# Optimization experiments

Hardware: AMD Instinct MI355X
Metric: run time of the kernel (lower is better)

Reference implementation:

```python
import jax, jax.numpy as jnp
import numpy as np

B, C_IN, H, W = 4, 128, 32, 32
C_SKIP, C_OUT = 64, 64
D_MODEL = 2 * C_SKIP            # 128 (channels after concat)
D_STATE, D_CONV, EXPAND = 16, 4, 2
D_INNER = EXPAND * D_MODEL      # 256
DT_RANK = int(np.ceil(D_MODEL / 16))  # 8
LN_EPS = 1e-5


def setup_inputs() -> dict:
    key = jax.random.key(0)
    ks = jax.random.split(key, 12)
    s = 0.02
    return {
        "x": jax.random.normal(ks[0], (B, C_IN, H, W), jnp.float32),
        "skip_x": jax.random.normal(ks[1], (B, C_SKIP, 2 * H, 2 * W), jnp.float32),
        # ConvTranspose2d(in, skip, k=2, s=2): torch weight layout (in, out, kh, kw)
        "up_w": jax.random.normal(ks[2], (C_IN, C_SKIP, 2, 2), jnp.float32) * s,
        "up_b": jnp.zeros((C_SKIP,), jnp.float32),
        # Mamba params (torch Linear layout: (out_features, in_features))
        "in_proj_w": jax.random.normal(ks[3], (2 * D_INNER, D_MODEL), jnp.float32) * s,
        "conv1d_w": jax.random.normal(ks[4], (D_INNER, 1, D_CONV), jnp.float32) * s,
        "conv1d_b": jnp.zeros((D_INNER,), jnp.float32),
        "x_proj_w": jax.random.normal(ks[5], (DT_RANK + 2 * D_STATE, D_INNER), jnp.float32) * s,
        "dt_proj_w": jax.random.normal(ks[6], (D_INNER, DT_RANK), jnp.float32) * s,
        "dt_proj_b": jnp.zeros((D_INNER,), jnp.float32),
        "A_log": jnp.log(jnp.broadcast_to(jnp.arange(1, D_STATE + 1, dtype=jnp.float32), (D_INNER, D_STATE))),
        "Dp": jnp.ones((D_INNER,), jnp.float32),
        "out_proj_w": jax.random.normal(ks[7], (D_MODEL, D_INNER), jnp.float32) * s,
        "ln_gamma": jnp.ones((D_MODEL,), jnp.float32),
        "ln_beta": jnp.zeros((D_MODEL,), jnp.float32),
        # Conv2d 1x1 (out, in)
        "convout_w": jax.random.normal(ks[8], (C_OUT, D_MODEL), jnp.float32) * s,
        "convout_b": jnp.zeros((C_OUT,), jnp.float32),
    }


def _selective_scan(u, delta, A, Bm, Cm, Dp):
    # u, delta: (B,L,Din); A: (Din,Ds); Bm, Cm: (B,L,Ds)
    deltaA = jnp.exp(delta[..., None] * A)                        # (B,L,Din,Ds)
    deltaBu = delta[..., None] * Bm[:, :, None, :] * u[..., None]  # (B,L,Din,Ds)

    def step(h, xs):
        dA, dBu, c = xs                 # (B,Din,Ds),(B,Din,Ds),(B,Ds)
        h = dA * h + dBu
        y = jnp.einsum('bdn,bn->bd', h, c)
        return h, y

    h0 = jnp.zeros((u.shape[0], D_INNER, D_STATE), u.dtype)
    xs = (deltaA.transpose(1, 0, 2, 3), deltaBu.transpose(1, 0, 2, 3), Cm.transpose(1, 0, 2))
    _, ys = jax.lax.scan(step, h0, xs)  # (L,B,Din)
    return ys.transpose(1, 0, 2) + u * Dp


def _mamba(seq, in_proj_w, conv1d_w, conv1d_b, x_proj_w, dt_proj_w, dt_proj_b, A_log, Dp, out_proj_w):
    # seq: (B, L, D_MODEL)
    xz = seq @ in_proj_w.T                      # (B,L,2*Din)
    u, z = jnp.split(xz, 2, axis=-1)
    # depthwise causal conv1d along L
    uc = u.transpose(0, 2, 1)                   # (B,Din,L)
    uc = jax.lax.conv_general_dilated(
        uc, conv1d_w, window_strides=(1,), padding=[(D_CONV - 1, 0)],
        feature_group_count=D_INNER, dimension_numbers=('NCH', 'OIH', 'NCH'))
    uc = uc + conv1d_b[None, :, None]
    u = jax.nn.silu(uc.transpose(0, 2, 1))      # (B,L,Din)
    dbc = u @ x_proj_w.T                        # (B,L,DT_RANK+2*Ds)
    dt, Bm, Cm = jnp.split(dbc, [DT_RANK, DT_RANK + D_STATE], axis=-1)
    delta = jax.nn.softplus(dt @ dt_proj_w.T + dt_proj_b)
    A = -jnp.exp(A_log)
    y = _selective_scan(u, delta, A, Bm, Cm, Dp)
    y = y * jax.nn.silu(z)
    return y @ out_proj_w.T                     # (B,L,D_MODEL)


def reference(x, skip_x, up_w, up_b, in_proj_w, conv1d_w, conv1d_b, x_proj_w,
              dt_proj_w, dt_proj_b, A_log, Dp, out_proj_w, ln_gamma, ln_beta,
              convout_w, convout_b):
    b, _, h, w = x.shape
    # ConvTranspose2d k=2 s=2: each pixel expands to a 2x2 block
    up = jnp.einsum('bchw,coij->bohiwj', x, up_w).reshape(b, C_SKIP, 2 * h, 2 * w)
    up = up + up_b[None, :, None, None]
    xc = jnp.concatenate([up, skip_x], axis=1)  # (B, D_MODEL, 2H, 2W)
    Hh, Ww = xc.shape[2], xc.shape[3]
    seq = xc.reshape(b, D_MODEL, Hh * Ww).transpose(0, 2, 1)  # (B,L,D)
    y = _mamba(seq, in_proj_w, conv1d_w, conv1d_b, x_proj_w, dt_proj_w,
               dt_proj_b, A_log, Dp, out_proj_w)
    xm = y.transpose(0, 2, 1).reshape(b, D_MODEL, Hh, Ww)
    # permute -> LayerNorm over channels -> permute back
    xn = xm.transpose(0, 2, 3, 1)
    mu = xn.mean(-1, keepdims=True)
    var = xn.var(-1, keepdims=True)
    xn = (xn - mu) * jax.lax.rsqrt(var + LN_EPS) * ln_gamma + ln_beta
    xm = jax.nn.silu(xn.transpose(0, 3, 1, 2))
    out = jnp.einsum('bchw,oc->bohw', xm, convout_w) + convout_b[None, :, None, None]
    return out
```

## Files before the change

kernel.cpp:

```cpp
#include <hip/hip_runtime.h>

#define L_SEQ 4096
#define DM 128
#define DIN 256
#define NC 128
#define CHUNK 32

__global__ __launch_bounds__(256) void upcat_kernel(
    const float* __restrict__ x, const float* __restrict__ skip,
    const float* __restrict__ up_w, const float* __restrict__ up_b,
    float* __restrict__ seq) {
  int b = blockIdx.x >> 6, hh = blockIdx.x & 63;
  int h = hh >> 1, i = hh & 1;
  int tid = threadIdx.x;
  __shared__ float xs[128][32];
  __shared__ float wsh[2][128][64];
  for (int e = tid; e < 1024; e += 256) {
    int c = e >> 3, q = e & 7;
    *(float4*)&xs[c][q * 4] =
        *(const float4*)(x + (((size_t)b * 128 + c) * 32 + h) * 32 + q * 4);
  }
  for (int e = tid; e < 8192; e += 256) {
    int c = e >> 6, o = e & 63;
    float2 v = *(const float2*)(up_w + c * 256 + o * 4 + i * 2);
    wsh[0][c][o] = v.x;
    wsh[1][c][o] = v.y;
  }
  __syncthreads();
  int tx = tid & 15, ty = tid >> 4;
  float4 bv = *(const float4*)(up_b + tx * 4);
  float acc[4][4];
#pragma unroll
  for (int a = 0; a < 4; ++a) {
    acc[a][0] = bv.x; acc[a][1] = bv.y; acc[a][2] = bv.z; acc[a][3] = bv.w;
  }
#pragma unroll 4
  for (int c = 0; c < 128; ++c) {
    float x0 = xs[c][ty * 2];
    float x1 = xs[c][ty * 2 + 1];
    float4 w0 = *(const float4*)&wsh[0][c][tx * 4];
    float4 w1 = *(const float4*)&wsh[1][c][tx * 4];
    acc[0][0] = fmaf(x0, w0.x, acc[0][0]); acc[0][1] = fmaf(x0, w0.y, acc[0][1]);
    acc[0][2] = fmaf(x0, w0.z, acc[0][2]); acc[0][3] = fmaf(x0, w0.w, acc[0][3]);
    acc[1][0] = fmaf(x0, w1.x, acc[1][0]); acc[1][1] = fmaf(x0, w1.y, acc[1][1]);
    acc[1][2] = fmaf(x0, w1.z, acc[1][2]); acc[1][3] = fmaf(x0, w1.w, acc[1][3]);
    acc[2][0] = fmaf(x1, w0.x, acc[2][0]); acc[2][1] = fmaf(x1, w0.y, acc[2][1]);
    acc[2][2] = fmaf(x1, w0.z, acc[2][2]); acc[2][3] = fmaf(x1, w0.w, acc[2][3]);
    acc[3][0] = fmaf(x1, w1.x, acc[3][0]); acc[3][1] = fmaf(x1, w1.y, acc[3][1]);
    acc[3][2] = fmaf(x1, w1.z, acc[3][2]); acc[3][3] = fmaf(x1, w1.w, acc[3][3]);
  }
  size_t mrow_base = (size_t)b * L_SEQ + (size_t)hh * 64;
#pragma unroll
  for (int a = 0; a < 4; ++a) {
    int ww = ty * 4 + a;
    *(float4*)(seq + (mrow_base + ww) * DM + tx * 4) =
        make_float4(acc[a][0], acc[a][1], acc[a][2], acc[a][3]);
  }
  for (int e = tid; e < 4096; e += 256) {
    int c = e & 63, ww = e >> 6;
    seq[(mrow_base + ww) * DM + 64 + c] =
        skip[((size_t)b * 64 + c) * (size_t)L_SEQ + hh * 64 + ww];
  }
}

__global__ __launch_bounds__(256) void gemm_bt(
    const float* __restrict__ A, const float* __restrict__ W,
    float* __restrict__ C, int M, int N, int K) {
  __shared__ float As[32][68];
  __shared__ float Ws[32][68];
  int m0 = blockIdx.x * 64, n0 = blockIdx.y * 64;
  int tid = threadIdx.x;
  int tx = tid & 15, ty = tid >> 4;
  float acc[4][4];
#pragma unroll
  for (int a = 0; a < 4; ++a)
#pragma unroll
    for (int bb = 0; bb < 4; ++bb) acc[a][bb] = 0.f;

  for (int k0 = 0; k0 < K; k0 += 32) {
    __syncthreads();
    for (int e = tid; e < 512; e += 256) {
      int r = e >> 3;
      int c4 = (e & 7) << 2;
      float4 va = *(const float4*)(A + (size_t)(m0 + r) * K + k0 + c4);
      As[c4 + 0][r] = va.x; As[c4 + 1][r] = va.y;
      As[c4 + 2][r] = va.z; As[c4 + 3][r] = va.w;
      float4 vw = *(const float4*)(W + (size_t)(n0 + r) * K + k0 + c4);
      Ws[c4 + 0][r] = vw.x; Ws[c4 + 1][r] = vw.y;
      Ws[c4 + 2][r] = vw.z; Ws[c4 + 3][r] = vw.w;
    }
    __syncthreads();
#pragma unroll
    for (int kk = 0; kk < 32; ++kk) {
      float4 av = *(const float4*)(&As[kk][ty * 4]);
      float4 wv = *(const float4*)(&Ws[kk][tx * 4]);
      float av_[4] = {av.x, av.y, av.z, av.w};
      float wv_[4] = {wv.x, wv.y, wv.z, wv.w};
#pragma unroll
      for (int a = 0; a < 4; ++a)
#pragma unroll
        for (int bb = 0; bb < 4; ++bb)
          acc[a][bb] = fmaf(av_[a], wv_[bb], acc[a][bb]);
    }
  }
#pragma unroll
  for (int a = 0; a < 4; ++a)
#pragma unroll
    for (int bb = 0; bb < 4; ++bb)
      C[(size_t)(m0 + ty * 4 + a) * N + n0 + tx * 4 + bb] = acc[a][bb];
}

__global__ __launch_bounds__(256) void conv_silu_kernel(
    const float* __restrict__ xz, const float* __restrict__ cw,
    const float* __restrict__ cb, float* __restrict__ u) {
  int idx = blockIdx.x * 256 + threadIdx.x;
  int d = idx & 255;
  int m = idx >> 8;
  int l = m & (L_SEQ - 1);
  float acc = cb[d];
#pragma unroll
  for (int t = 0; t < 4; ++t) {
    int ls = l - 3 + t;
    if (ls >= 0)
      acc = fmaf(xz[(size_t)(m - 3 + t) * 512 + d], cw[d * 4 + t], acc);
  }
  u[idx] = acc / (1.f + __expf(-acc));
}

__global__ __launch_bounds__(256) void xproj_kernel(
    const float* __restrict__ u, const float* __restrict__ W,
    float* __restrict__ dbc) {
  __shared__ float us[64][68];
  int m0 = blockIdx.x * 64;
  int tid = threadIdx.x;
  int lane = tid & 63;
  int w = __builtin_amdgcn_readfirstlane(tid >> 6);
  int jbase = blockIdx.y * 20 + w * 5;
  const float* Wb = W + jbase * 256;
  float acc[5];
#pragma unroll
  for (int j = 0; j < 5; ++j) acc[j] = 0.f;
  for (int k0 = 0; k0 < 256; k0 += 64) {
    __syncthreads();
    for (int e = tid; e < 1024; e += 256) {
      int r = e >> 4, q = e & 15;
      float4 v = *(const float4*)(u + (size_t)(m0 + r) * 256 + k0 + q * 4);
      *(float4*)&us[r][q * 4] = v;
    }
    __syncthreads();
#pragma unroll
    for (int kk = 0; kk < 64; kk += 4) {
      float4 a4 = *(const float4*)&us[lane][kk];
      float a_[4] = {a4.x, a4.y, a4.z, a4.w};
#pragma unroll
      for (int i = 0; i < 4; ++i)
#pragma unroll
        for (int j = 0; j < 5; ++j)
          acc[j] = fmaf(a_[i], Wb[j * 256 + k0 + kk + i], acc[j]);
    }
  }
  size_t base = (size_t)(m0 + lane) * 40 + jbase;
#pragma unroll
  for (int j = 0; j < 5; ++j) dbc[base + j] = acc[j];
}


__device__ __forceinline__ float softplus_f(float a) {
  return (a > 20.f) ? a : log1pf(__expf(a));
}

__global__ __launch_bounds__(256) void scan_pass1(
    const float* __restrict__ u, const float* __restrict__ dbc,
    const float* __restrict__ A_log, const float* __restrict__ Wdt,
    const float* __restrict__ bdt, float* __restrict__ carryA,
    float* __restrict__ carryH) {
  int bid = blockIdx.x;
  int b = bid >> 7;
  int c = bid & (NC - 1);
  int d = threadIdx.x;
  __shared__ float ls[CHUNK * 40];
  size_t l0 = (size_t)b * L_SEQ + (size_t)c * CHUNK;
  const float* rp = dbc + l0 * 40;
  for (int e = d; e < CHUNK * 40; e += 256) ls[e] = rp[e];
  float Ac[16];
  {
    const float4* ar = (const float4*)(A_log + d * 16);
#pragma unroll
    for (int q = 0; q < 4; ++q) {
      float4 v = ar[q];
      Ac[q * 4 + 0] = -__expf(v.x); Ac[q * 4 + 1] = -__expf(v.y);
      Ac[q * 4 + 2] = -__expf(v.z); Ac[q * 4 + 3] = -__expf(v.w);
    }
  }
  float wdt[8];
  {
    const float4* wr = (const float4*)(Wdt + d * 8);
    float4 v0 = wr[0], v1 = wr[1];
    wdt[0] = v0.x; wdt[1] = v0.y; wdt[2] = v0.z; wdt[3] = v0.w;
    wdt[4] = v1.x; wdt[5] = v1.y; wdt[6] = v1.z; wdt[7] = v1.w;
  }
  float bdt_v = bdt[d];
  const float* up = u + l0 * 256 + d;
  __syncthreads();
  float h[16];
#pragma unroll
  for (int n = 0; n < 16; ++n) h[n] = 0.f;
  float dvs = 0.f;
#pragma unroll 4
  for (int li = 0; li < CHUNK; ++li) {
    float uv = up[(size_t)li * 256];
    float acc = bdt_v;
#pragma unroll
    for (int j = 0; j < 8; ++j)
      acc = fmaf(ls[li * 40 + j], wdt[j], acc);
    float dv = softplus_f(acc);
    dvs += dv;
    float t = dv * uv;
#pragma unroll
    for (int n = 0; n < 16; ++n) {
      float dA = __expf(dv * Ac[n]);
      h[n] = fmaf(dA, h[n], t * ls[li * 40 + 8 + n]);
    }
  }
  float4* cA = (float4*)(carryA + ((size_t)bid * 256 + d) * 16);
  float4* cH = (float4*)(carryH + ((size_t)bid * 256 + d) * 16);
#pragma unroll
  for (int q = 0; q < 4; ++q) {
    cA[q] = make_float4(__expf(dvs * Ac[q * 4]), __expf(dvs * Ac[q * 4 + 1]),
                        __expf(dvs * Ac[q * 4 + 2]), __expf(dvs * Ac[q * 4 + 3]));
    cH[q] = make_float4(h[q * 4], h[q * 4 + 1], h[q * 4 + 2], h[q * 4 + 3]);
  }
}

__global__ __launch_bounds__(256) void scan_mid(
    const float* __restrict__ carryA, float* __restrict__ carryH) {
  int gid = blockIdx.x * 256 + threadIdx.x;
  int b = gid >> 12;
  int dn = gid & 4095;
  float h = 0.f;
  for (int c = 0; c < NC; ++c) {
    size_t i = ((size_t)(b * NC + c) << 12) + dn;
    float a = carryA[i];
    float hl = carryH[i];
    carryH[i] = h;
    h = fmaf(a, h, hl);
  }
}

__global__ __launch_bounds__(256) void scan_pass3(
    const float* __restrict__ u, const float* __restrict__ dbc,
    const float* __restrict__ xz, const float* __restrict__ A_log,
    const float* __restrict__ Wdt, const float* __restrict__ bdt,
    const float* __restrict__ Dp, const float* __restrict__ carryH,
    float* __restrict__ y) {
  int bid = blockIdx.x;
  int b = bid >> 7;
  int c = bid & (NC - 1);
  int d = threadIdx.x;
  __shared__ float ls[CHUNK * 40];
  size_t l0 = (size_t)b * L_SEQ + (size_t)c * CHUNK;
  const float* rp = dbc + l0 * 40;
  for (int e = d; e < CHUNK * 40; e += 256) ls[e] = rp[e];
  float Ac[16];
  {
    const float4* ar = (const float4*)(A_log + d * 16);
#pragma unroll
    for (int q = 0; q < 4; ++q) {
      float4 v = ar[q];
      Ac[q * 4 + 0] = -__expf(v.x); Ac[q * 4 + 1] = -__expf(v.y);
      Ac[q * 4 + 2] = -__expf(v.z); Ac[q * 4 + 3] = -__expf(v.w);
    }
  }
  float wdt[8];
  {
    const float4* wr = (const float4*)(Wdt + d * 8);
    float4 v0 = wr[0], v1 = wr[1];
    wdt[0] = v0.x; wdt[1] = v0.y; wdt[2] = v0.z; wdt[3] = v0.w;
    wdt[4] = v1.x; wdt[5] = v1.y; wdt[6] = v1.z; wdt[7] = v1.w;
  }
  float bdt_v = bdt[d];
  float Dv = Dp[d];
  float h[16];
  {
    const float4* cH = (const float4*)(carryH + ((size_t)bid * 256 + d) * 16);
#pragma unroll
    for (int q = 0; q < 4; ++q) {
      float4 v = cH[q];
      h[q * 4 + 0] = v.x; h[q * 4 + 1] = v.y;
      h[q * 4 + 2] = v.z; h[q * 4 + 3] = v.w;
    }
  }
  const float* up = u + l0 * 256 + d;
  const float* zp = xz + l0 * 512 + 256 + d;
  float* yp = y + l0 * 256 + d;
  __syncthreads();
#pragma unroll 4
  for (int li = 0; li < CHUNK; ++li) {
    float uv = up[(size_t)li * 256];
    float zv = zp[(size_t)li * 512];
    float acc = bdt_v;
#pragma unroll
    for (int j = 0; j < 8; ++j)
      acc = fmaf(ls[li * 40 + j], wdt[j], acc);
    float dv = softplus_f(acc);
    float t = dv * uv;
    float p = 0.f;
#pragma unroll
    for (int n = 0; n < 16; ++n) {
      float dA = __expf(dv * Ac[n]);
      h[n] = fmaf(dA, h[n], t * ls[li * 40 + 8 + n]);
      p = fmaf(h[n], ls[li * 40 + 24 + n], p);
    }
    float s = zv / (1.f + __expf(-zv));
    yp[(size_t)li * 256] = (p + uv * Dv) * s;
  }
}

__global__ __launch_bounds__(256) void ln_out_kernel(
    const float* __restrict__ s2, const float* __restrict__ gamma,
    const float* __restrict__ beta, const float* __restrict__ Wo,
    const float* __restrict__ bo, float* __restrict__ out) {
  __shared__ float xt[64][129];
  __shared__ float mus[64], invs[64];
  int tid = threadIdx.x;
  int m0 = blockIdx.x * 64;
  for (int i = 0; i < 8; ++i) {
    int s = tid + i * 256;
    int r = s >> 5, q = s & 31;
    float4 v = *(const float4*)(s2 + (size_t)(m0 + r) * 128 + q * 4);
    xt[r][q * 4 + 0] = v.x; xt[r][q * 4 + 1] = v.y;
    xt[r][q * 4 + 2] = v.z; xt[r][q * 4 + 3] = v.w;
  }
  __syncthreads();
  {
    int r = tid >> 2, kq = (tid & 3) * 32;
    float s = 0.f, q = 0.f;
#pragma unroll 8
    for (int kk = 0; kk < 32; ++kk) {
      float v = xt[r][kq + kk];
      s += v; q = fmaf(v, v, q);
    }
    s += __shfl_xor(s, 1, 64); s += __shfl_xor(s, 2, 64);
    q += __shfl_xor(q, 1, 64); q += __shfl_xor(q, 2, 64);
    if ((tid & 3) == 0) {
      float mu = s * (1.f / 128.f);
      float var = q * (1.f / 128.f) - mu * mu;
      mus[r] = mu;
      invs[r] = rsqrtf(var + 1e-5f);
    }
  }
  __syncthreads();
  for (int i = 0; i < 32; ++i) {
    int idx = tid + i * 256;
    int r = idx >> 7, k = idx & 127;
    float v = xt[r][k];
    float xn = (v - mus[r]) * invs[r] * gamma[k] + beta[k];
    xt[r][k] = xn / (1.f + __expf(-xn));
  }
  __syncthreads();
  int lane = tid & 63;
  int w = __builtin_amdgcn_readfirstlane(tid >> 6);
  int cbase = blockIdx.y * 32 + w * 8;
  const float* Wrow = Wo + cbase * 128;
  float acc[8];
#pragma unroll
  for (int j = 0; j < 8; ++j) acc[j] = 0.f;
#pragma unroll 4
  for (int k = 0; k < 128; ++k) {
    float v = xt[lane][k];
#pragma unroll
    for (int j = 0; j < 8; ++j)
      acc[j] = fmaf(v, Wrow[j * 128 + k], acc[j]);
  }
  int m = m0 + lane;
  int b = m >> 12, l = m & 4095;
#pragma unroll
  for (int j = 0; j < 8; ++j)
    out[((size_t)b * 64 + cbase + j) * 4096 + l] = acc[j] + bo[cbase + j];
}

extern "C" void kernel_launch(void* const* d_in, const int* in_sizes, int n_in,
                              void* d_out, int out_size, void* d_ws, size_t ws_size,
                              hipStream_t stream) {
  (void)in_sizes; (void)n_in; (void)out_size; (void)ws_size;
  const float* x         = (const float*)d_in[0];
  const float* skip      = (const float*)d_in[1];
  const float* up_w      = (const float*)d_in[2];
  const float* up_b      = (const float*)d_in[3];
  const float* in_proj_w = (const float*)d_in[4];
  const float* conv1d_w  = (const float*)d_in[5];
  const float* conv1d_b  = (const float*)d_in[6];
  const float* x_proj_w  = (const float*)d_in[7];
  const float* dt_proj_w = (const float*)d_in[8];
  const float* dt_proj_b = (const float*)d_in[9];
  const float* A_log     = (const float*)d_in[10];
  const float* Dp        = (const float*)d_in[11];
  const float* out_proj_w= (const float*)d_in[12];
  const float* ln_gamma  = (const float*)d_in[13];
  const float* ln_beta   = (const float*)d_in[14];
  const float* convout_w = (const float*)d_in[15];
  const float* convout_b = (const float*)d_in[16];
  float* out = (float*)d_out;
  float* ws  = (float*)d_ws;

  float* seq    = ws;
  float* xz     = ws + 2097152;
  float* u      = ws + 10485760;
  float* dbc    = ws + 14680064;
  float* y      = ws + 15335424;
  float* carryA = ws + 19529728;
  float* carryH = ws + 21626880;

  upcat_kernel<<<256, 256, 0, stream>>>(x, skip, up_w, up_b, seq);
  gemm_bt<<<dim3(16384 / 64, 512 / 64), 256, 0, stream>>>(seq, in_proj_w, xz,
                                                          16384, 512, 128);
  conv_silu_kernel<<<16384, 256, 0, stream>>>(xz, conv1d_w, conv1d_b, u);
  xproj_kernel<<<dim3(16384 / 64, 2), 256, 0, stream>>>(u, x_proj_w, dbc);
  scan_pass1<<<4 * NC, 256, 0, stream>>>(u, dbc, A_log, dt_proj_w, dt_proj_b,
                                         carryA, carryH);
  scan_mid<<<64, 256, 0, stream>>>(carryA, carryH);
  scan_pass3<<<4 * NC, 256, 0, stream>>>(u, dbc, xz, A_log, dt_proj_w,
                                         dt_proj_b, Dp, carryH, y);
  gemm_bt<<<dim3(16384 / 64, 128 / 64), 256, 0, stream>>>(y, out_proj_w, seq,
                                                          16384, 128, 256);
  ln_out_kernel<<<dim3(256, 2), 256, 0, stream>>>(seq, ln_gamma, ln_beta,
                                                  convout_w, convout_b, out);
}
```

Measured before the change: 204.8 us.

## Fuse depthwise conv+SiLU into x_proj kernel and use 128-row in_proj GEMM tile

Removes the standalone conv_silu kernel by computing the causal depthwise conv and SiLU inside the x_proj kernel from a shared-memory tile of xz with a 3-row halo, and writes u from one of the two y-blocks. The in_proj GEMM switches to a new 128x64 tile variant with 8x4 per-thread accumulators. This saves a kernel launch and a full read of xz plus a re-read of u. The cost is that the conv is computed twice (once per blockIdx.y) and the larger tile uses more registers.

After: 193.5 us (median of 2 runs). -5.5%, faster.

```diff
diff --git a/kernel.cpp b/kernel.cpp
--- a/kernel.cpp
+++ b/kernel.cpp
@@ -63,6 +63,56 @@
   }
 }
 
+__global__ __launch_bounds__(256) void gemm_bt128(
+    const float* __restrict__ A, const float* __restrict__ W,
+    float* __restrict__ C, int M, int N, int K) {
+  __shared__ float As[32][132];
+  __shared__ float Ws[32][68];
+  int m0 = blockIdx.x * 128, n0 = blockIdx.y * 64;
+  int tid = threadIdx.x;
+  int tx = tid & 15, ty = tid >> 4;
+  float acc[8][4];
+#pragma unroll
+  for (int a = 0; a < 8; ++a)
+#pragma unroll
+    for (int bb = 0; bb < 4; ++bb) acc[a][bb] = 0.f;
+
+  for (int k0 = 0; k0 < K; k0 += 32) {
+    __syncthreads();
+    for (int e = tid; e < 1024; e += 256) {
+      int r = e >> 3, c4 = (e & 7) << 2;
+      float4 va = *(const float4*)(A + (size_t)(m0 + r) * K + k0 + c4);
+      As[c4 + 0][r] = va.x; As[c4 + 1][r] = va.y;
+      As[c4 + 2][r] = va.z; As[c4 + 3][r] = va.w;
+    }
+    for (int e = tid; e < 512; e += 256) {
+      int r = e >> 3, c4 = (e & 7) << 2;
+      float4 vw = *(const float4*)(W + (size_t)(n0 + r) * K + k0 + c4);
+      Ws[c4 + 0][r] = vw.x; Ws[c4 + 1][r] = vw.y;
+      Ws[c4 + 2][r] = vw.z; Ws[c4 + 3][r] = vw.w;
+    }
+    __syncthreads();
+#pragma unroll
+    for (int kk = 0; kk < 32; ++kk) {
+      float4 a0 = *(const float4*)(&As[kk][ty * 8]);
+      float4 a1 = *(const float4*)(&As[kk][ty * 8 + 4]);
+      float4 wv = *(const float4*)(&Ws[kk][tx * 4]);
+      float a_[8] = {a0.x, a0.y, a0.z, a0.w, a1.x, a1.y, a1.z, a1.w};
+      float w_[4] = {wv.x, wv.y, wv.z, wv.w};
+#pragma unroll
+      for (int a = 0; a < 8; ++a)
+#pragma unroll
+        for (int bb = 0; bb < 4; ++bb)
+          acc[a][bb] = fmaf(a_[a], w_[bb], acc[a][bb]);
+    }
+  }
+#pragma unroll
+  for (int a = 0; a < 8; ++a)
+#pragma unroll
+    for (int bb = 0; bb < 4; ++bb)
+      C[(size_t)(m0 + ty * 8 + a) * N + n0 + tx * 4 + bb] = acc[a][bb];
+}
+
 __global__ __launch_bounds__(256) void gemm_bt(
     const float* __restrict__ A, const float* __restrict__ W,
     float* __restrict__ C, int M, int N, int K) {
@@ -110,26 +160,11 @@
       C[(size_t)(m0 + ty * 4 + a) * N + n0 + tx * 4 + bb] = acc[a][bb];
 }
 
-__global__ __launch_bounds__(256) void conv_silu_kernel(
+__global__ __launch_bounds__(256) void xproj_kernel(
     const float* __restrict__ xz, const float* __restrict__ cw,
-    const float* __restrict__ cb, float* __restrict__ u) {
-  int idx = blockIdx.x * 256 + threadIdx.x;
-  int d = idx & 255;
-  int m = idx >> 8;
-  int l = m & (L_SEQ - 1);
-  float acc = cb[d];
-#pragma unroll
-  for (int t = 0; t < 4; ++t) {
-    int ls = l - 3 + t;
-    if (ls >= 0)
-      acc = fmaf(xz[(size_t)(m - 3 + t) * 512 + d], cw[d * 4 + t], acc);
-  }
-  u[idx] = acc / (1.f + __expf(-acc));
-}
-
-__global__ __launch_bounds__(256) void xproj_kernel(
-    const float* __restrict__ u, const float* __restrict__ W,
-    float* __restrict__ dbc) {
+    const float* __restrict__ cb, const float* __restrict__ W,
+    float* __restrict__ dbc, float* __restrict__ u_out) {
+  __shared__ float xzt[67][64];
   __shared__ float us[64][68];
   int m0 = blockIdx.x * 64;
   int tid = threadIdx.x;
@@ -137,15 +172,60 @@
   int w = __builtin_amdgcn_readfirstlane(tid >> 6);
   int jbase = blockIdx.y * 20 + w * 5;
   const float* Wb = W + jbase * 256;
+  bool first = (m0 & (L_SEQ - 1)) == 0;
+  int cc4 = (tid & 15) << 2;
+  int r0 = tid >> 4;
   float acc[5];
 #pragma unroll
   for (int j = 0; j < 5; ++j) acc[j] = 0.f;
   for (int k0 = 0; k0 < 256; k0 += 64) {
     __syncthreads();
-    for (int e = tid; e < 1024; e += 256) {
-      int r = e >> 4, q = e & 15;
-      float4 v = *(const float4*)(u + (size_t)(m0 + r) * 256 + k0 + q * 4);
-      *(float4*)&us[r][q * 4] = v;
+    for (int e = tid; e < 67 * 16; e += 256) {
+      int rr = e >> 4, c4 = (e & 15) << 2;
+      float4 v;
+      if (first && rr < 3)
+        v = make_float4(0.f, 0.f, 0.f, 0.f);
+      else
+        v = *(const float4*)(xz + (size_t)(m0 - 3 + rr) * 512 + k0 + c4);
+      *(float4*)&xzt[rr][c4] = v;
+    }
+    __syncthreads();
+    {
+      int d = k0 + cc4;
+      float4 cw0 = *(const float4*)(cw + (d + 0) * 4);
+      float4 cw1 = *(const float4*)(cw + (d + 1) * 4);
+      float4 cw2 = *(const float4*)(cw + (d + 2) * 4);
+      float4 cw3 = *(const float4*)(cw + (d + 3) * 4);
+      float4 cbv = *(const float4*)(cb + d);
+#pragma unroll
+      for (int s = 0; s < 4; ++s) {
+        int r = r0 + s * 16;
+        float a0 = cbv.x, a1 = cbv.y, a2 = cbv.z, a3 = cbv.w;
+        a0 = fmaf(xzt[r + 0][cc4 + 0], cw0.x, a0);
+        a0 = fmaf(xzt[r + 1][cc4 + 0], cw0.y, a0);
+        a0 = fmaf(xzt[r + 2][cc4 + 0], cw0.z, a0);
+        a0 = fmaf(xzt[r + 3][cc4 + 0], cw0.w, a0);
+        a1 = fmaf(xzt[r + 0][cc4 + 1], cw1.x, a1);
+        a1 = fmaf(xzt[r + 1][cc4 + 1], cw1.y, a1);
+        a1 = fmaf(xzt[r + 2][cc4 + 1], cw1.z, a1);
+        a1 = fmaf(xzt[r + 3][cc4 + 1], cw1.w, a1);
+        a2 = fmaf(xzt[r + 0][cc4 + 2], cw2.x, a2);
+        a2 = fmaf(xzt[r + 1][cc4 + 2], cw2.y, a2);
+        a2 = fmaf(xzt[r + 2][cc4 + 2], cw2.z, a2);
+        a2 = fmaf(xzt[r + 3][cc4 + 2], cw2.w, a2);
+        a3 = fmaf(xzt[r + 0][cc4 + 3], cw3.x, a3);
+        a3 = fmaf(xzt[r + 1][cc4 + 3], cw3.y, a3);
+        a3 = fmaf(xzt[r + 2][cc4 + 3], cw3.z, a3);
+        a3 = fmaf(xzt[r + 3][cc4 + 3], cw3.w, a3);
+        float o0 = a0 / (1.f + __expf(-a0));
+        float o1 = a1 / (1.f + __expf(-a1));
+        float o2 = a2 / (1.f + __expf(-a2));
+        float o3 = a3 / (1.f + __expf(-a3));
+        *(float4*)&us[r][cc4] = make_float4(o0, o1, o2, o3);
+        if (blockIdx.y == 0)
+          *(float4*)(u_out + (size_t)(m0 + r) * 256 + d) =
+              make_float4(o0, o1, o2, o3);
+      }
     }
     __syncthreads();
 #pragma unroll
@@ -163,7 +243,6 @@
 #pragma unroll
   for (int j = 0; j < 5; ++j) dbc[base + j] = acc[j];
 }
-
 
 __device__ __forceinline__ float softplus_f(float a) {
   return (a > 20.f) ? a : log1pf(__expf(a));
@@ -412,10 +491,10 @@
   float* carryH = ws + 21626880;
 
   upcat_kernel<<<256, 256, 0, stream>>>(x, skip, up_w, up_b, seq);
-  gemm_bt<<<dim3(16384 / 64, 512 / 64), 256, 0, stream>>>(seq, in_proj_w, xz,
-                                                          16384, 512, 128);
-  conv_silu_kernel<<<16384, 256, 0, stream>>>(xz, conv1d_w, conv1d_b, u);
-  xproj_kernel<<<dim3(16384 / 64, 2), 256, 0, stream>>>(u, x_proj_w, dbc);
+  gemm_bt128<<<dim3(16384 / 128, 512 / 64), 256, 0, stream>>>(
+      seq, in_proj_w, xz, 16384, 512, 128);
+  xproj_kernel<<<dim3(16384 / 64, 2), 256, 0, stream>>>(
+      xz, conv1d_w, conv1d_b, x_proj_w, dbc, u);
   scan_pass1<<<4 * NC, 256, 0, stream>>>(u, dbc, A_log, dt_proj_w, dt_proj_b,
                                          carryA, carryH);
   scan_mid<<<64, 256, 0, stream>>>(carryA, carryH);
```
